# Performance work log

Measured on AMD Instinct MI355X. Metric: run time of the kernel, lower is better.

Reference implementation:

```python
import jax, jax.numpy as jnp
import numpy as np

N, E, D, H, C = 50000, 800000, 64, 2, 64


def setup_inputs() -> dict:
    key = jax.random.key(0)
    ks = jax.random.split(key, 16)
    sc = 1.0 / np.sqrt(D)
    return {
        "left_features": jax.random.normal(ks[0], (N, D), jnp.float32),
        "edge_index": jax.random.randint(ks[1], (2, E), 0, N, jnp.int32),
        "edge_features": jax.random.normal(ks[2], (E, D), jnp.float32),
        "right_features": jax.random.normal(ks[3], (N, D), jnp.float32),
        "scatter_out_size": N,
        # GATConv params (shared lin for src/dst since in_channels is int)
        "W_lin": jax.random.normal(ks[4], (D, H * C), jnp.float32) * sc,
        "att_src": jax.random.normal(ks[5], (H, C), jnp.float32) * sc,
        "att_dst": jax.random.normal(ks[6], (H, C), jnp.float32) * sc,
        "W_edge": jax.random.normal(ks[7], (D, H * C), jnp.float32) * sc,
        "att_edge": jax.random.normal(ks[8], (H, C), jnp.float32) * sc,
        "bias_conv": jnp.zeros((H * C,), jnp.float32),
        # trailing dense layers
        "W_lt": jax.random.normal(ks[9], (H * C, C), jnp.float32) * sc,
        "b_lt": jnp.zeros((C,), jnp.float32),
        "W_fm": jax.random.normal(ks[10], (C, C), jnp.float32) * sc,
        "b_fm": jnp.zeros((C,), jnp.float32),
        "W_pc": jax.random.normal(ks[11], (2 * C, C), jnp.float32) * sc,
        "b_pc": jnp.zeros((C,), jnp.float32),
    }


def reference(left_features, edge_index, edge_features, right_features,
              scatter_out_size, W_lin, att_src, att_dst, W_edge, att_edge,
              bias_conv, W_lt, b_lt, W_fm, b_fm, W_pc, b_pc):
    src, dst = edge_index[0], edge_index[1]
    Nl = scatter_out_size
    # linear projections to [*, H, C]
    x_src = (right_features @ W_lin).reshape(-1, H, C)
    x_dst = (left_features @ W_lin).reshape(-1, H, C)
    # per-node attention logits [*, H]
    a_src = (x_src * att_src).sum(-1)
    a_dst = (x_dst * att_dst).sum(-1)
    e_feat = (edge_features @ W_edge).reshape(-1, H, C)
    a_edge = (e_feat * att_edge).sum(-1)  # [E, H]
    # per-edge logits, leaky relu, segment softmax over dst neighborhoods
    alpha = a_src[src] + a_dst[dst] + a_edge  # [E, H]
    alpha = jax.nn.leaky_relu(alpha, negative_slope=0.2)
    m = jax.ops.segment_max(alpha, dst, num_segments=Nl)
    m = jnp.where(jnp.isfinite(m), m, 0.0)  # empty segments -> 0
    ex = jnp.exp(alpha - m[dst])
    s = jax.ops.segment_sum(ex, dst, num_segments=Nl)
    att = ex / (s[dst] + 1e-16)  # [E, H]
    # weighted message scatter-sum, concat heads
    msg = x_src[src] * att[:, :, None]  # [E, H, C]
    out = jax.ops.segment_sum(msg, dst, num_segments=Nl).reshape(Nl, H * C)
    out = out + bias_conv
    # trailing dense chain
    x = jax.nn.relu(out) @ W_lt + b_lt          # linear_transform
    x = jax.nn.relu(x) @ W_fm + b_fm            # feature_module_final
    left_updated = jnp.concatenate([left_features, x], axis=-1) @ W_pc + b_pc
    return left_updated, edge_index, att
```

## Files before the change

kernel.cpp:

```cpp
#include <hip/hip_runtime.h>
#include <hip/hip_bf16.h>

typedef unsigned int uint32;
typedef unsigned short ushort16;
typedef float f32x4 __attribute__((ext_vector_type(4)));
typedef short bf16x8 __attribute__((ext_vector_type(8)));

#define HH 2
#define CC 64
#define DD 64
#define HC 128

__device__ __forceinline__ float bf2f(ushort16 u) {
    union { float f; uint32 u; } x; x.u = ((uint32)u) << 16; return x.f;
}
__device__ __forceinline__ ushort16 f2bf(float f) {
    union { float f; uint32 u; } x; x.f = f;
    uint32 u = x.u;
    u += 0x7FFFu + ((u >> 16) & 1u);
    return (ushort16)(u >> 16);
}
__device__ __forceinline__ int clampi(int v, int N) {
    return min(max(v, 0), N - 1);
}
__device__ __forceinline__ void cvt_hilo8(const float* x, bf16x8& hi, bf16x8& lo) {
    #pragma unroll
    for (int i = 0; i < 8; i++) {
        union { float f; uint32 u; } a; a.f = x[i];
        uint32 uh = a.u & 0xFFFF0000u;
        hi[i] = (short)(uh >> 16);
        union { float f; uint32 u; } hf; hf.u = uh;
        lo[i] = (short)f2bf(a.f - hf.f);
    }
}

__global__ void k_fold(const float* W_lin, const float* att_src,
                       const float* att_dst, const float* W_edge,
                       const float* att_edge, float* vfold) {
    int t = threadIdx.x;
    int h = t >> 6, d = t & 63;
    float vs = 0.f, vd = 0.f, ve = 0.f;
    for (int c = 0; c < CC; c++) {
        float wl = W_lin[d * HC + h * CC + c];
        vs += wl * att_src[h * CC + c];
        vd += wl * att_dst[h * CC + c];
        ve += W_edge[d * HC + h * CC + c] * att_edge[h * CC + c];
    }
    vfold[t] = vs; vfold[128 + t] = vd; vfold[256 + t] = ve;
}

__global__ __launch_bounds__(256) void k_node_logits(
    const float* right, const float* left, const float* vfold,
    float* a_src, float* a_dst, int N)
{
    __shared__ float vs[HC], vd[HC];
    if (threadIdx.x < HC) {
        vs[threadIdx.x] = vfold[threadIdx.x];
        vd[threadIdx.x] = vfold[HC + threadIdx.x];
    }
    __syncthreads();
    int n = blockIdx.x * 256 + threadIdx.x;
    if (n >= N) return;
    const float4* rr = (const float4*)(right + (size_t)n * DD);
    const float4* lr = (const float4*)(left  + (size_t)n * DD);
    float p0 = 0.f, p1 = 0.f, q0 = 0.f, q1 = 0.f;
    #pragma unroll
    for (int i = 0; i < 16; i++) {
        float4 r4 = rr[i], l4 = lr[i];
        float4 s0 = *(const float4*)&vs[i * 4];
        float4 s1 = *(const float4*)&vs[64 + i * 4];
        float4 d0 = *(const float4*)&vd[i * 4];
        float4 d1 = *(const float4*)&vd[64 + i * 4];
        p0 += r4.x * s0.x + r4.y * s0.y + r4.z * s0.z + r4.w * s0.w;
        p1 += r4.x * s1.x + r4.y * s1.y + r4.z * s1.z + r4.w * s1.w;
        q0 += l4.x * d0.x + l4.y * d0.y + l4.z * d0.z + l4.w * d0.w;
        q1 += l4.x * d1.x + l4.y * d1.y + l4.z * d1.z + l4.w * d1.w;
    }
    *(float2*)(a_src + (size_t)n * 2) = make_float2(p0, p1);
    *(float2*)(a_dst + (size_t)n * 2) = make_float2(q0, q1);
}

__global__ __launch_bounds__(256) void k_edge_alpha(
    const float* edge_feat, const int* ei, const float* vfold,
    const float* a_src, const float* a_dst,
    float* att_slot, int* counts, int E, int N)
{
    __shared__ float vE[HC];
    if (threadIdx.x < HC) vE[threadIdx.x] = vfold[256 + threadIdx.x];
    __syncthreads();
    int e = blockIdx.x * 256 + threadIdx.x;
    if (e >= E) return;
    const float4* row = (const float4*)(edge_feat + (size_t)e * DD);
    float p0 = 0.f, p1 = 0.f;
    #pragma unroll
    for (int i = 0; i < 16; i++) {
        float4 f = row[i];
        float4 w0 = *(const float4*)&vE[i * 4];
        float4 w1 = *(const float4*)&vE[64 + i * 4];
        p0 += f.x * w0.x + f.y * w0.y + f.z * w0.z + f.w * w0.w;
        p1 += f.x * w1.x + f.y * w1.y + f.z * w1.z + f.w * w1.w;
    }
    int s  = clampi(ei[e], N);
    int d2 = clampi(ei[E + e], N);
    float2 asr = *(const float2*)(a_src + (size_t)s * 2);
    float2 ads = *(const float2*)(a_dst + (size_t)d2 * 2);
    float al0 = asr.x + ads.x + p0;
    float al1 = asr.y + ads.y + p1;
    al0 = (al0 > 0.f) ? al0 : 0.2f * al0;
    al1 = (al1 > 0.f) ? al1 : 0.2f * al1;
    *(float2*)(att_slot + (size_t)e * 2) = make_float2(al0, al1);
    atomicAdd(&counts[d2], 1);
}

__global__ void k_scan1(const int* counts, int* bsum, int N) {
    int idx = blockIdx.x * 256 + threadIdx.x;
    int v = (idx < N) ? counts[idx] : 0;
    #pragma unroll
    for (int m = 32; m >= 1; m >>= 1) v += __shfl_xor(v, m, 64);
    __shared__ int wsum[4];
    if ((threadIdx.x & 63) == 0) wsum[threadIdx.x >> 6] = v;
    __syncthreads();
    if (threadIdx.x == 0) bsum[blockIdx.x] = wsum[0] + wsum[1] + wsum[2] + wsum[3];
}

__global__ void k_scan2(const int* bsum, int* bpre, int NB) {
    __shared__ int sh[256];
    int t = threadIdx.x;
    int v = (t < NB) ? bsum[t] : 0;
    sh[t] = v;
    __syncthreads();
    for (int off = 1; off < 256; off <<= 1) {
        int add = (t >= off) ? sh[t - off] : 0;
        __syncthreads();
        sh[t] += add;
        __syncthreads();
    }
    if (t < NB) bpre[t] = sh[t] - v;
}

__global__ void k_scan3(const int* counts, const int* bpre,
                        int* offs, int* cursor, int N) {
    __shared__ int sh[256];
    int t = threadIdx.x;
    int idx = blockIdx.x * 256 + t;
    int v = (idx < N) ? counts[idx] : 0;
    sh[t] = v;
    __syncthreads();
    for (int off = 1; off < 256; off <<= 1) {
        int add = (t >= off) ? sh[t - off] : 0;
        __syncthreads();
        sh[t] += add;
        __syncthreads();
    }
    if (idx < N) {
        int ex = bpre[blockIdx.x] + sh[t] - v;
        offs[idx] = ex;
        cursor[idx] = ex;
    }
}

__global__ void k_ids(const int* ei, int* cursor, int* sorted, int E, int N) {
    int e = blockIdx.x * 256 + threadIdx.x;
    if (e >= E) return;
    int d = clampi(ei[E + e], N);
    int pos = atomicAdd(&cursor[d], 1);
    sorted[pos] = e;
}

__global__ __launch_bounds__(256) void k_gather(
    const int* ei, const int* offs, const int* counts, const int* sorted,
    const float* right, float* att_slot, float* agg, int N)
{
    int w = threadIdx.x >> 6, lane = threadIdx.x & 63;
    for (int n = blockIdx.x * 4 + w; n < N; n += gridDim.x * 4) {
        int start = offs[n], deg = counts[n];
        float m0 = -1e30f, m1 = -1e30f;
        for (int i = lane; i < deg; i += 64) {
            int e = sorted[start + i];
            m0 = fmaxf(m0, att_slot[e * 2]);
            m1 = fmaxf(m1, att_slot[e * 2 + 1]);
        }
        #pragma unroll
        for (int m = 32; m >= 1; m >>= 1) {
            m0 = fmaxf(m0, __shfl_xor(m0, m, 64));
            m1 = fmaxf(m1, __shfl_xor(m1, m, 64));
        }
        float s0 = 0.f, s1 = 0.f, acc0 = 0.f, acc1 = 0.f;
        for (int base = 0; base < deg; base += 64) {
            int cnt = min(deg - base, 64);
            float ex0 = 0.f, ex1 = 0.f; int src = 0;
            if (lane < cnt) {
                int e = sorted[start + base + lane];
                ex0 = __expf(att_slot[e * 2]     - m0);
                ex1 = __expf(att_slot[e * 2 + 1] - m1);
                src = clampi(ei[e], N);
            }
            float t0 = ex0, t1 = ex1;
            #pragma unroll
            for (int m = 32; m >= 1; m >>= 1) {
                t0 += __shfl_xor(t0, m, 64); t1 += __shfl_xor(t1, m, 64);
            }
            s0 += t0; s1 += t1;
            for (int i = 0; i < cnt; i++) {
                float w0 = __shfl(ex0, i, 64);
                float w1 = __shfl(ex1, i, 64);
                int   si = __shfl(src, i, 64);
                float v = right[(size_t)si * DD + lane];
                acc0 += w0 * v; acc1 += w1 * v;
            }
        }
        float inv0 = 1.f / (s0 + 1e-16f), inv1 = 1.f / (s1 + 1e-16f);
        for (int i = lane; i < deg; i += 64) {
            int e = sorted[start + i];
            att_slot[e * 2]     = __expf(att_slot[e * 2]     - m0) * inv0;
            att_slot[e * 2 + 1] = __expf(att_slot[e * 2 + 1] - m1) * inv1;
        }
        agg[(size_t)n * HC + lane]      = acc0 * inv0;
        agg[(size_t)n * HC + 64 + lane] = acc1 * inv1;
    }
}

__global__ __launch_bounds__(256) void k_lin_mfma(
    const float* __restrict__ W_lin, const float* __restrict__ bc,
    float* agg, int N)
{
    __shared__ __align__(16) ushort16 sW[16][512];
    __shared__ float sB[HC];
    for (int t = threadIdx.x; t < 16 * 64; t += 256) {
        int lane = t & 63, f = t >> 6;
        int nt = f & 3, kt = (f >> 2) & 1, h = f >> 3;
        int n = h * CC + nt * 16 + (lane & 15);
        int k0 = kt * 32 + (lane >> 4) * 8;
        #pragma unroll
        for (int i = 0; i < 8; i++)
            sW[f][lane * 8 + i] = f2bf(W_lin[(size_t)(k0 + i) * HC + n]);
    }
    if (threadIdx.x < HC) sB[threadIdx.x] = bc[threadIdx.x];
    __syncthreads();
    int w = threadIdx.x >> 6, lane = threadIdx.x & 63;
    int lhi = lane >> 4, llo = lane & 15;
    int tiles = (N + 63) >> 6;
    for (int tile = blockIdx.x; tile < tiles; tile += gridDim.x) {
        int nb = tile * 64 + w * 16;
        int arow = min(nb + llo, N - 1);
        const float* ap = agg + (size_t)arow * HC;
        bf16x8 Ah[2][2], Al[2][2];
        #pragma unroll
        for (int h = 0; h < 2; h++)
            #pragma unroll
            for (int kt = 0; kt < 2; kt++) {
                float x8[8];
                *(f32x4*)&x8[0] = *(const f32x4*)(ap + h * 64 + kt * 32 + lhi * 8);
                *(f32x4*)&x8[4] = *(const f32x4*)(ap + h * 64 + kt * 32 + lhi * 8 + 4);
                cvt_hilo8(x8, Ah[h][kt], Al[h][kt]);
            }
        f32x4 acc[2][4];
        #pragma unroll
        for (int h = 0; h < 2; h++)
            #pragma unroll
            for (int nt = 0; nt < 4; nt++) {
                float b = sB[h * 64 + nt * 16 + llo];
                acc[h][nt][0] = b; acc[h][nt][1] = b;
                acc[h][nt][2] = b; acc[h][nt][3] = b;
            }
        #pragma unroll
        for (int h = 0; h < 2; h++)
            #pragma unroll
            for (int kt = 0; kt < 2; kt++)
                #pragma unroll
                for (int nt = 0; nt < 4; nt++) {
                    bf16x8 b = *(const bf16x8*)&sW[h * 8 + kt * 4 + nt][lane * 8];
                    acc[h][nt] = __builtin_amdgcn_mfma_f32_16x16x32_bf16(Al[h][kt], b, acc[h][nt], 0, 0, 0);
                    acc[h][nt] = __builtin_amdgcn_mfma_f32_16x16x32_bf16(Ah[h][kt], b, acc[h][nt], 0, 0, 0);
                }
        #pragma unroll
        for (int h = 0; h < 2; h++)
            #pragma unroll
            for (int nt = 0; nt < 4; nt++)
                #pragma unroll
                for (int j = 0; j < 4; j++) {
                    int node = nb + 4 * lhi + j;
                    if (node < N)
                        agg[(size_t)node * HC + h * 64 + nt * 16 + llo] =
                            fmaxf(acc[h][nt][j], 0.f);
                }
    }
}

__global__ __launch_bounds__(256) void k_tail_mfma(
    const float* __restrict__ t0, const float* __restrict__ left,
    const float* __restrict__ W_lt, const float* __restrict__ b_lt,
    const float* __restrict__ W_fm, const float* __restrict__ b_fm,
    const float* __restrict__ W_pc, const float* __restrict__ b_pc,
    float* __restrict__ out, int N)
{
    __shared__ __align__(16) ushort16 sWlt[16][512];
    __shared__ __align__(16) ushort16 sWfm[8][512];
    __shared__ __align__(16) ushort16 sWpT[8][512];
    __shared__ __align__(16) ushort16 sWpB[8][512];
    __shared__ __align__(16) float sX[4][1024];
    __shared__ float sblt[CC], sbfm[CC], sbpc[CC];
    for (int t = threadIdx.x; t < 16 * 64; t += 256) {
        int lane = t & 63, f = t >> 6, nt = f & 3, kt = f >> 2;
        int n = nt * 16 + (lane & 15), k0 = kt * 32 + (lane >> 4) * 8;
        #pragma unroll
        for (int i = 0; i < 8; i++)
            sWlt[f][lane * 8 + i] = f2bf(W_lt[(k0 + i) * CC + n]);
    }
    for (int t = threadIdx.x; t < 8 * 64; t += 256) {
        int lane = t & 63, f = t >> 6, nt = f & 3, kt = f >> 2;
        int n = nt * 16 + (lane & 15), k0 = kt * 32 + (lane >> 4) * 8;
        #pragma unroll
        for (int i = 0; i < 8; i++) {
            sWfm[f][lane * 8 + i] = f2bf(W_fm[(k0 + i) * CC + n]);
            sWpT[f][lane * 8 + i] = f2bf(W_pc[(k0 + i) * CC + n]);
            sWpB[f][lane * 8 + i] = f2bf(W_pc[(64 + k0 + i) * CC + n]);
        }
    }
    if (threadIdx.x < CC) {
        sblt[threadIdx.x] = b_lt[threadIdx.x];
        sbfm[threadIdx.x] = b_fm[threadIdx.x];
        sbpc[threadIdx.x] = b_pc[threadIdx.x];
    }
    __syncthreads();
    int w = threadIdx.x >> 6, lane = threadIdx.x & 63;
    int lhi = lane >> 4, llo = lane & 15;
    float* xw = &sX[w][0];
    int swz = (llo & 7) << 2;
    int tiles = (N + 63) >> 6;
    for (int tile = blockIdx.x; tile < tiles; tile += gridDim.x) {
        int nb = tile * 64 + w * 16;
        int arow = min(nb + llo, N - 1);
        f32x4 acc2[4];
        #pragma unroll
        for (int nt = 0; nt < 4; nt++) {
            float b = sblt[nt * 16 + llo];
            acc2[nt][0] = b; acc2[nt][1] = b; acc2[nt][2] = b; acc2[nt][3] = b;
        }
        const float* tp = t0 + (size_t)arow * HC;
        #pragma unroll
        for (int kt = 0; kt < 4; kt++) {
            float x8[8];
            *(f32x4*)&x8[0] = *(const f32x4*)(tp + kt * 32 + lhi * 8);
            *(f32x4*)&x8[4] = *(const f32x4*)(tp + kt * 32 + lhi * 8 + 4);
            bf16x8 ah, al; cvt_hilo8(x8, ah, al);
            #pragma unroll
            for (int nt = 0; nt < 4; nt++) {
                bf16x8 b = *(const bf16x8*)&sWlt[kt * 4 + nt][lane * 8];
                acc2[nt] = __builtin_amdgcn_mfma_f32_16x16x32_bf16(al, b, acc2[nt], 0, 0, 0);
                acc2[nt] = __builtin_amdgcn_mfma_f32_16x16x32_bf16(ah, b, acc2[nt], 0, 0, 0);
            }
        }
        #pragma unroll
        for (int nt = 0; nt < 4; nt++)
            #pragma unroll
            for (int j = 0; j < 4; j++) {
                int row = 4 * lhi + j, col = nt * 16 + llo;
                xw[row * 64 + (col ^ ((row & 7) << 2))] = fmaxf(acc2[nt][j], 0.f);
            }
        f32x4 acc3[4];
        #pragma unroll
        for (int nt = 0; nt < 4; nt++) {
            float b = sbfm[nt * 16 + llo];
            acc3[nt][0] = b; acc3[nt][1] = b; acc3[nt][2] = b; acc3[nt][3] = b;
        }
        #pragma unroll
        for (int kt = 0; kt < 2; kt++) {
            int k0 = kt * 32 + lhi * 8;
            float x8[8];
            *(f32x4*)&x8[0] = *(const f32x4*)&xw[llo * 64 + ((k0    ) ^ swz)];
            *(f32x4*)&x8[4] = *(const f32x4*)&xw[llo * 64 + ((k0 + 4) ^ swz)];
            bf16x8 ah, al; cvt_hilo8(x8, ah, al);
            #pragma unroll
            for (int nt = 0; nt < 4; nt++) {
                bf16x8 b = *(const bf16x8*)&sWfm[kt * 4 + nt][lane * 8];
                acc3[nt] = __builtin_amdgcn_mfma_f32_16x16x32_bf16(al, b, acc3[nt], 0, 0, 0);
                acc3[nt] = __builtin_amdgcn_mfma_f32_16x16x32_bf16(ah, b, acc3[nt], 0, 0, 0);
            }
        }
        #pragma unroll
        for (int nt = 0; nt < 4; nt++)
            #pragma unroll
            for (int j = 0; j < 4; j++) {
                int row = 4 * lhi + j, col = nt * 16 + llo;
                xw[row * 64 + (col ^ ((row & 7) << 2))] = acc3[nt][j];
            }
        f32x4 acc4[4];
        #pragma unroll
        for (int nt = 0; nt < 4; nt++) {
            float b = sbpc[nt * 16 + llo];
            acc4[nt][0] = b; acc4[nt][1] = b; acc4[nt][2] = b; acc4[nt][3] = b;
        }
        const float* lp = left + (size_t)arow * DD;
        #pragma unroll
        for (int kt = 0; kt < 2; kt++) {
            float x8[8];
            *(f32x4*)&x8[0] = *(const f32x4*)(lp + kt * 32 + lhi * 8);
            *(f32x4*)&x8[4] = *(const f32x4*)(lp + kt * 32 + lhi * 8 + 4);
            bf16x8 ah, al; cvt_hilo8(x8, ah, al);
            #pragma unroll
            for (int nt = 0; nt < 4; nt++) {
                bf16x8 b = *(const bf16x8*)&sWpT[kt * 4 + nt][lane * 8];
                acc4[nt] = __builtin_amdgcn_mfma_f32_16x16x32_bf16(al, b, acc4[nt], 0, 0, 0);
                acc4[nt] = __builtin_amdgcn_mfma_f32_16x16x32_bf16(ah, b, acc4[nt], 0, 0, 0);
            }
        }
        #pragma unroll
        for (int kt = 0; kt < 2; kt++) {
            int k0 = kt * 32 + lhi * 8;
            float x8[8];
            *(f32x4*)&x8[0] = *(const f32x4*)&xw[llo * 64 + ((k0    ) ^ swz)];
            *(f32x4*)&x8[4] = *(const f32x4*)&xw[llo * 64 + ((k0 + 4) ^ swz)];
            bf16x8 ah, al; cvt_hilo8(x8, ah, al);
            #pragma unroll
            for (int nt = 0; nt < 4; nt++) {
                bf16x8 b = *(const bf16x8*)&sWpB[kt * 4 + nt][lane * 8];
                acc4[nt] = __builtin_amdgcn_mfma_f32_16x16x32_bf16(al, b, acc4[nt], 0, 0, 0);
                acc4[nt] = __builtin_amdgcn_mfma_f32_16x16x32_bf16(ah, b, acc4[nt], 0, 0, 0);
            }
        }
        #pragma unroll
        for (int nt = 0; nt < 4; nt++)
            #pragma unroll
            for (int j = 0; j < 4; j++) {
                int node = nb + 4 * lhi + j;
                if (node < N)
                    out[(size_t)node * CC + nt * 16 + llo] = acc4[nt][j];
            }
    }
}

__global__ void k_copy_idx(const int* ei, float* out, int n) {
    for (int i = blockIdx.x * blockDim.x + threadIdx.x; i < n;
         i += gridDim.x * blockDim.x)
        out[i] = (float)ei[i];
}

extern "C" void kernel_launch(void* const* d_in, const int* in_sizes, int n_in,
                              void* d_out, int out_size, void* d_ws, size_t ws_size,
                              hipStream_t stream) {
    const float* left      = (const float*)d_in[0];
    const int*   ei        = (const int*)d_in[1];
    const float* efeat     = (const float*)d_in[2];
    const float* right     = (const float*)d_in[3];
    const float* W_lin     = (const float*)d_in[5];
    const float* att_src   = (const float*)d_in[6];
    const float* att_dst   = (const float*)d_in[7];
    const float* W_edge    = (const float*)d_in[8];
    const float* att_edge  = (const float*)d_in[9];
    const float* bias_conv = (const float*)d_in[10];
    const float* W_lt      = (const float*)d_in[11];
    const float* b_lt      = (const float*)d_in[12];
    const float* W_fm      = (const float*)d_in[13];
    const float* b_fm      = (const float*)d_in[14];
    const float* W_pc      = (const float*)d_in[15];
    const float* b_pc      = (const float*)d_in[16];

    const int N = in_sizes[0] / DD;
    const int E = in_sizes[2] / DD;
    const int NB = (N + 255) / 256;

    float* ws     = (float*)d_ws;
    float* vfold  = ws;
    float* a_src  = ws + 512;
    float* a_dst  = a_src + 2 * (size_t)N;
    int*   counts = (int*)(a_dst + 2 * (size_t)N);
    int*   offs   = counts + N;
    int*   cursor = offs + N;
    int*   bsum   = cursor + N;
    int*   bpre   = bsum + 256;
    int*   sorted = bpre + 256;
    float* agg    = (float*)(sorted + E);
    (void)ws_size; (void)n_in; (void)out_size;

    float* out_lu   = (float*)d_out;
    float* out_ei   = out_lu + (size_t)N * CC;
    float* att_slot = out_ei + (size_t)2 * E;

    hipMemsetAsync(counts, 0, (size_t)N * sizeof(int), stream);

    hipLaunchKernelGGL(k_fold, dim3(1), dim3(128), 0, stream,
                       W_lin, att_src, att_dst, W_edge, att_edge, vfold);
    hipLaunchKernelGGL(k_node_logits, dim3((N + 255) / 256), dim3(256), 0, stream,
                       right, left, vfold, a_src, a_dst, N);
    hipLaunchKernelGGL(k_edge_alpha, dim3((E + 255) / 256), dim3(256), 0, stream,
                       efeat, ei, vfold, a_src, a_dst, att_slot, counts, E, N);
    hipLaunchKernelGGL(k_scan1, dim3(NB), dim3(256), 0, stream,
                       counts, bsum, N);
    hipLaunchKernelGGL(k_scan2, dim3(1), dim3(256), 0, stream,
                       bsum, bpre, NB);
    hipLaunchKernelGGL(k_scan3, dim3(NB), dim3(256), 0, stream,
                       counts, bpre, offs, cursor, N);
    hipLaunchKernelGGL(k_ids, dim3((E + 255) / 256), dim3(256), 0, stream,
                       ei, cursor, sorted, E, N);
    hipLaunchKernelGGL(k_gather, dim3((N + 3) / 4), dim3(256), 0, stream,
                       ei, offs, counts, sorted, right, att_slot, agg, N);
    hipLaunchKernelGGL(k_lin_mfma, dim3(512), dim3(256), 0, stream,
                       W_lin, bias_conv, agg, N);
    hipLaunchKernelGGL(k_tail_mfma, dim3(512), dim3(256), 0, stream,
                       agg, left, W_lt, b_lt, W_fm, b_fm, W_pc, b_pc, out_lu, N);
    hipLaunchKernelGGL(k_copy_idx, dim3(1024), dim3(256), 0, stream,
                       ei, out_ei, 2 * E);
}
```

Before: 554.4 us.

## Process four edges per wave in gather with float4 row loads

Restructures the per-node gather so each wavefront splits into four 16-lane groups, each handling a different edge and loading its 64-float source row as float4 vectors. Partial sums are then combined across groups with cross-lane shuffles. This removes the serial per-edge broadcast loop and its shuffles, and exposes more memory-level parallelism for low-degree nodes, where most lanes used to sit idle. Attention logits are also read and written as float2. In exchange, each group needs a final cross-group reduction and lanes in groups with no edge left sit idle on the tail iteration.

Measured after the change: 541.1 us. -2.4%, faster.

```diff
diff --git a/kernel.cpp b/kernel.cpp
--- a/kernel.cpp
+++ b/kernel.cpp
@@ -172,51 +172,61 @@
     const float* right, float* att_slot, float* agg, int N)
 {
     int w = threadIdx.x >> 6, lane = threadIdx.x & 63;
+    int g = lane >> 4, sub = lane & 15;
     for (int n = blockIdx.x * 4 + w; n < N; n += gridDim.x * 4) {
         int start = offs[n], deg = counts[n];
         float m0 = -1e30f, m1 = -1e30f;
         for (int i = lane; i < deg; i += 64) {
             int e = sorted[start + i];
-            m0 = fmaxf(m0, att_slot[e * 2]);
-            m1 = fmaxf(m1, att_slot[e * 2 + 1]);
+            float2 a = *(const float2*)(att_slot + (size_t)e * 2);
+            m0 = fmaxf(m0, a.x);
+            m1 = fmaxf(m1, a.y);
         }
         #pragma unroll
         for (int m = 32; m >= 1; m >>= 1) {
             m0 = fmaxf(m0, __shfl_xor(m0, m, 64));
             m1 = fmaxf(m1, __shfl_xor(m1, m, 64));
         }
-        float s0 = 0.f, s1 = 0.f, acc0 = 0.f, acc1 = 0.f;
-        for (int base = 0; base < deg; base += 64) {
-            int cnt = min(deg - base, 64);
-            float ex0 = 0.f, ex1 = 0.f; int src = 0;
-            if (lane < cnt) {
-                int e = sorted[start + base + lane];
-                ex0 = __expf(att_slot[e * 2]     - m0);
-                ex1 = __expf(att_slot[e * 2 + 1] - m1);
-                src = clampi(ei[e], N);
-            }
-            float t0 = ex0, t1 = ex1;
-            #pragma unroll
-            for (int m = 32; m >= 1; m >>= 1) {
-                t0 += __shfl_xor(t0, m, 64); t1 += __shfl_xor(t1, m, 64);
-            }
-            s0 += t0; s1 += t1;
-            for (int i = 0; i < cnt; i++) {
-                float w0 = __shfl(ex0, i, 64);
-                float w1 = __shfl(ex1, i, 64);
-                int   si = __shfl(src, i, 64);
-                float v = right[(size_t)si * DD + lane];
-                acc0 += w0 * v; acc1 += w1 * v;
-            }
+        float s0 = 0.f, s1 = 0.f;
+        f32x4 acc0 = {0.f, 0.f, 0.f, 0.f}, acc1 = {0.f, 0.f, 0.f, 0.f};
+        for (int base = 0; base < deg; base += 4) {
+            int i = base + g;
+            if (i < deg) {
+                int e = sorted[start + i];
+                float2 a = *(const float2*)(att_slot + (size_t)e * 2);
+                float ex0 = __expf(a.x - m0);
+                float ex1 = __expf(a.y - m1);
+                int si = clampi(ei[e], N);
+                f32x4 v = *(const f32x4*)(right + (size_t)si * DD + sub * 4);
+                acc0 += ex0 * v;
+                acc1 += ex1 * v;
+                s0 += ex0; s1 += ex1;
+            }
+        }
+        s0 += __shfl_xor(s0, 16, 64); s0 += __shfl_xor(s0, 32, 64);
+        s1 += __shfl_xor(s1, 16, 64); s1 += __shfl_xor(s1, 32, 64);
+        #pragma unroll
+        for (int j = 0; j < 4; j++) {
+            acc0[j] += __shfl_xor(acc0[j], 16, 64);
+            acc0[j] += __shfl_xor(acc0[j], 32, 64);
+            acc1[j] += __shfl_xor(acc1[j], 16, 64);
+            acc1[j] += __shfl_xor(acc1[j], 32, 64);
         }
         float inv0 = 1.f / (s0 + 1e-16f), inv1 = 1.f / (s1 + 1e-16f);
         for (int i = lane; i < deg; i += 64) {
             int e = sorted[start + i];
-            att_slot[e * 2]     = __expf(att_slot[e * 2]     - m0) * inv0;
-            att_slot[e * 2 + 1] = __expf(att_slot[e * 2 + 1] - m1) * inv1;
-        }
-        agg[(size_t)n * HC + lane]      = acc0 * inv0;
-        agg[(size_t)n * HC + 64 + lane] = acc1 * inv1;
+            float2 a = *(const float2*)(att_slot + (size_t)e * 2);
+            a.x = __expf(a.x - m0) * inv0;
+            a.y = __expf(a.y - m1) * inv1;
+            *(float2*)(att_slot + (size_t)e * 2) = a;
+        }
+        if (g == 0) {
+            f32x4 o = acc0 * inv0;
+            *(f32x4*)(agg + (size_t)n * HC + sub * 4) = o;
+        } else if (g == 1) {
+            f32x4 o = acc1 * inv1;
+            *(f32x4*)(agg + (size_t)n * HC + 64 + sub * 4) = o;
+        }
     }
 }
 
```
